# Optimization experiments

Measured on AMD Instinct MI355X. Metric: run time of the kernel, lower is better.

## Reference

```python
import jax, jax.numpy as jnp
import numpy as np

NUM_HEADS = 8
BLOCK = 16
EPS = 1e-5


def setup_inputs() -> dict:
    key = jax.random.key(0)
    ks = jax.random.split(key, 5)
    B, C, H, W = 2, 256, 192, 192
    x = jax.random.normal(ks[0], (B, C, H, W), dtype=jnp.float32)
    s = 1.0 / np.sqrt(C).astype(np.float32)
    Wq = jax.random.normal(ks[1], (C, C), dtype=jnp.float32) * s
    Wk = jax.random.normal(ks[2], (C, C), dtype=jnp.float32) * s
    Wv = jax.random.normal(ks[3], (C, C), dtype=jnp.float32) * s
    Wo = jax.random.normal(ks[4], (C, C), dtype=jnp.float32) * s
    gamma = jnp.ones((C,), dtype=jnp.float32)
    beta = jnp.zeros((C,), dtype=jnp.float32)
    return {"x": x, "Wq": Wq, "Wk": Wk, "Wv": Wv, "Wo": Wo, "gamma": gamma, "beta": beta}


def _to_blocks(t, B, nH, d, H, W, bs):
    # [B, C, H, W] -> [B, nH, n_blocks, bs*bs, d]
    nbh, nbw = H // bs, W // bs
    t = t.reshape(B, nH, d, nbh, bs, nbw, bs)
    t = t.transpose(0, 1, 3, 5, 4, 6, 2)  # B nH nbh nbw bs bs d
    return t.reshape(B, nH, nbh * nbw, bs * bs, d)


def _from_blocks(t, B, nH, d, H, W, bs):
    # [B, nH, n_blocks, bs*bs, d] -> [B, C, H, W]
    nbh, nbw = H // bs, W // bs
    t = t.reshape(B, nH, nbh, nbw, bs, bs, d)
    t = t.transpose(0, 1, 6, 2, 4, 3, 5)  # B nH d nbh bs nbw bs
    return t.reshape(B, nH * d, H, W)


def reference(x, Wq, Wk, Wv, Wo, gamma, beta):
    B, C, H, W = x.shape
    nH, bs = NUM_HEADS, BLOCK
    d = C // nH
    scale = 1.0 / np.float32(np.sqrt(d))

    # 1x1 convs == channel matmuls
    q = jnp.einsum('bchw,oc->bohw', x, Wq)
    k = jnp.einsum('bchw,oc->bohw', x, Wk)
    v = jnp.einsum('bchw,oc->bohw', x, Wv)

    qb = _to_blocks(q, B, nH, d, H, W, bs)
    kb = _to_blocks(k, B, nH, d, H, W, bs)
    vb = _to_blocks(v, B, nH, d, H, W, bs)

    # block-local attention: i,j index the bs*bs pixels inside a block
    scores = jnp.einsum('bnkid,bnkjd->bnkij', qb, kb) * scale
    attn = jax.nn.softmax(scores, axis=-1)
    o = jnp.einsum('bnkij,bnkjd->bnkid', attn, vb)

    o = _from_blocks(o, B, nH, d, H, W, bs)
    o = jnp.einsum('bchw,oc->bohw', o, Wo) + x  # output projection + residual

    # LayerNorm over channels
    mu = jnp.mean(o, axis=1, keepdims=True)
    var = jnp.var(o, axis=1, keepdims=True)
    o = (o - mu) * jax.lax.rsqrt(var + EPS)
    return o * gamma[None, :, None, None] + beta[None, :, None, None]
```

## Files before the change

### kernel.cpp

```cpp
#include <hip/hip_runtime.h>
#include <hip/hip_bf16.h>

namespace {

constexpr int kC    = 256;
constexpr int kH    = 192, kW = 192;
constexpr int kHW   = kH * kW;
constexpr int kNBD  = 12;
constexpr int kNBLK = kNBD * kNBD;

typedef __attribute__((ext_vector_type(8))) short          bf16x8;
typedef __attribute__((ext_vector_type(8))) unsigned short u16x8;
typedef __attribute__((ext_vector_type(4))) unsigned short u16x4;
typedef __attribute__((ext_vector_type(4))) float          f32x4;

__device__ __forceinline__ unsigned short f2bf(float f) {
  union { float f; unsigned u; } x; x.f = f;
  unsigned r = x.u + 0x7fffu + ((x.u >> 16) & 1u);
  return (unsigned short)(r >> 16);
}

__device__ __forceinline__ f32x4 mfma16(bf16x8 a, bf16x8 b, f32x4 c) {
  return __builtin_amdgcn_mfma_f32_16x16x32_bf16(a, b, c, 0, 0, 0);
}

__global__ void k_convw(const float* __restrict__ wq, const float* __restrict__ wk,
                        const float* __restrict__ wv, const float* __restrict__ wo,
                        unsigned short* __restrict__ dst) {
  int i = blockIdx.x * 256 + threadIdx.x;
  const float* s = (blockIdx.y == 0) ? wq : (blockIdx.y == 1) ? wk
                 : (blockIdx.y == 2) ? wv : wo;
  dst[(size_t)blockIdx.y * 65536 + i] = f2bf(s[i]);
}

__global__ __launch_bounds__(256, 3)
void k_qkv(const float* __restrict__ x, const unsigned short* __restrict__ wbf,
           unsigned short* __restrict__ qw, unsigned short* __restrict__ kw,
           unsigned short* __restrict__ vw) {
  __shared__ unsigned short xTs[64 * 256];
  __shared__ unsigned short oT[32 * 264];
  const int tid = threadIdx.x;
  const int w = tid >> 6, l = tid & 63;
  const int m0 = blockIdx.x * 64;
  const int b  = m0 / kHW;
  const int px0 = m0 % kHW;

  {
    const float* xb = x + (size_t)b * kC * kHW + px0;
    #pragma unroll
    for (int i = 0; i < 64; i += 2) {
      const int c = w * 64 + i;
      float f0 = xb[(size_t)c * kHW + l];
      float f1 = xb[(size_t)(c + 1) * kHW + l];
      unsigned pk = (unsigned)f2bf(f0) | ((unsigned)f2bf(f1) << 16);
      const int cb = c >> 3;
      const int col = ((cb ^ (l & 7)) << 3) + (c & 7);
      *(unsigned*)&xTs[l * 256 + col] = pk;
    }
  }
  __syncthreads();

  const int lane = tid & 63;
  const int l15 = lane & 15, l4 = lane >> 4;

  unsigned short* outs[3] = {qw, kw, vw};
  for (int mat = 0; mat < 3; ++mat) {
    const unsigned short* wmat = wbf + (size_t)mat * 65536;
    f32x4 acc[4][4];
    #pragma unroll
    for (int pt = 0; pt < 4; ++pt)
      #pragma unroll
      for (int ot = 0; ot < 4; ++ot)
        acc[pt][ot] = (f32x4){0.f, 0.f, 0.f, 0.f};

    for (int kc = 0; kc < 8; ++kc) {
      bf16x8 bfr[4];
      #pragma unroll
      for (int ot = 0; ot < 4; ++ot)
        bfr[ot] = *(const bf16x8*)&wmat[(size_t)(w * 64 + ot * 16 + l15) * 256 + kc * 32 + l4 * 8];
      #pragma unroll
      for (int pt = 0; pt < 4; ++pt) {
        const int cb = kc * 4 + l4;
        bf16x8 af = *(const bf16x8*)&xTs[(pt * 16 + l15) * 256 + ((cb ^ (l15 & 7)) << 3)];
        #pragma unroll
        for (int ot = 0; ot < 4; ++ot)
          acc[pt][ot] = mfma16(af, bfr[ot], acc[pt][ot]);
      }
    }
    unsigned short* dst = outs[mat] + ((size_t)b * kHW + px0) * 256;
    for (int half = 0; half < 2; ++half) {
      __syncthreads();
      #pragma unroll
      for (int pt2 = 0; pt2 < 2; ++pt2) {
        const int pt = half * 2 + pt2;
        #pragma unroll
        for (int ot = 0; ot < 4; ++ot)
          #pragma unroll
          for (int r = 0; r < 4; ++r)
            oT[(pt2 * 16 + l4 * 4 + r) * 264 + w * 64 + ot * 16 + l15] = f2bf(acc[pt][ot][r]);
      }
      __syncthreads();
      const int row = tid >> 3, ocb = tid & 7;
      #pragma unroll
      for (int k2 = 0; k2 < 4; ++k2) {
        u16x8 vv = *(const u16x8*)&oT[row * 264 + ocb * 32 + k2 * 8];
        *(u16x8*)&dst[(size_t)(half * 32 + row) * 256 + ocb * 32 + k2 * 8] = vv;
      }
    }
  }
}

__global__ __launch_bounds__(512, 2)
void k_attn(const unsigned short* __restrict__ qw, const unsigned short* __restrict__ kw,
            const unsigned short* __restrict__ vw, unsigned short* __restrict__ ow) {
  __shared__ unsigned short P[256][264];
  __shared__ unsigned short T[32][264];
  const int tid = threadIdx.x;
  int bx = blockIdx.x;
  const int blk = bx % kNBLK; bx /= kNBLK;
  const int head = bx & 7; const int b = bx >> 3;
  const int bh = blk / kNBD, bw = blk % kNBD;
  const int px00 = bh * 16 * kW + bw * 16;
  const size_t base = ((size_t)b * kHW) * 256 + head * 32;

  {
    const int j = tid >> 1, half = tid & 1;
    const int px = px00 + (j >> 4) * kW + (j & 15);
    const unsigned short* vp = vw + base + (size_t)px * 256 + half * 16;
    u16x8 a = *(const u16x8*)&vp[0];
    u16x8 c = *(const u16x8*)&vp[8];
    #pragma unroll
    for (int e = 0; e < 8; ++e) {
      T[half * 16 + e][j]     = a[e];
      T[half * 16 + 8 + e][j] = c[e];
    }
  }

  const int lane = tid & 63, wave = tid >> 6;
  const int l15 = lane & 15, l4 = lane >> 4;
  const f32x4 fz = {0.f, 0.f, 0.f, 0.f};

  bf16x8 qfr[2];
  #pragma unroll
  for (int it = 0; it < 2; ++it) {
    const int i  = wave * 32 + it * 16 + l15;
    const int px = px00 + (i >> 4) * kW + (i & 15);
    qfr[it] = *(const bf16x8*)&qw[base + (size_t)px * 256 + l4 * 8];
  }
  f32x4 s[16][2];
  #pragma unroll
  for (int jt = 0; jt < 16; ++jt) {
    const int px = px00 + jt * kW + l15;
    bf16x8 kf = *(const bf16x8*)&kw[base + (size_t)px * 256 + l4 * 8];
    s[jt][0] = mfma16(kf, qfr[0], fz);
    s[jt][1] = mfma16(kf, qfr[1], fz);
  }

  const float sc = 0.17677669529663687f;
  #pragma unroll
  for (int it = 0; it < 2; ++it) {
    float m = -3.0e38f;
    #pragma unroll
    for (int jt = 0; jt < 16; ++jt)
      #pragma unroll
      for (int r = 0; r < 4; ++r)
        m = fmaxf(m, s[jt][it][r]);
    m = fmaxf(m, __shfl_xor(m, 16));
    m = fmaxf(m, __shfl_xor(m, 32));
    float su = 0.f;
    #pragma unroll
    for (int jt = 0; jt < 16; ++jt)
      #pragma unroll
      for (int r = 0; r < 4; ++r) {
        float e = __expf((s[jt][it][r] - m) * sc);
        s[jt][it][r] = e;
        su += e;
      }
    su += __shfl_xor(su, 16);
    su += __shfl_xor(su, 32);
    const float inv = 1.f / su;
    const int i = wave * 32 + it * 16 + l15;
    #pragma unroll
    for (int jt = 0; jt < 16; ++jt) {
      u16x4 pk;
      #pragma unroll
      for (int r = 0; r < 4; ++r) pk[r] = f2bf(s[jt][it][r] * inv);
      *(u16x4*)&P[i][jt * 16 + l4 * 4] = pk;
    }
  }
  __syncthreads();

  f32x4 oa[2][2];
  oa[0][0] = fz; oa[0][1] = fz; oa[1][0] = fz; oa[1][1] = fz;
  #pragma unroll
  for (int kt = 0; kt < 8; ++kt) {
    bf16x8 av0 = *(const bf16x8*)&T[l15][kt * 32 + l4 * 8];
    bf16x8 av1 = *(const bf16x8*)&T[16 + l15][kt * 32 + l4 * 8];
    bf16x8 bp0 = *(const bf16x8*)&P[wave * 32 + l15][kt * 32 + l4 * 8];
    bf16x8 bp1 = *(const bf16x8*)&P[wave * 32 + 16 + l15][kt * 32 + l4 * 8];
    oa[0][0] = mfma16(av0, bp0, oa[0][0]);
    oa[0][1] = mfma16(av0, bp1, oa[0][1]);
    oa[1][0] = mfma16(av1, bp0, oa[1][0]);
    oa[1][1] = mfma16(av1, bp1, oa[1][1]);
  }
  __syncthreads();
  #pragma unroll
  for (int ddt = 0; ddt < 2; ++ddt)
    #pragma unroll
    for (int it = 0; it < 2; ++it)
      #pragma unroll
      for (int r = 0; r < 4; ++r)
        T[ddt * 16 + l4 * 4 + r][wave * 32 + it * 16 + l15] = f2bf(oa[ddt][it][r]);
  __syncthreads();
  {
    const int i = tid >> 1, half = tid & 1;
    const int px = px00 + (i >> 4) * kW + (i & 15);
    u16x8 w0, w1;
    #pragma unroll
    for (int e = 0; e < 8; ++e) {
      w0[e] = T[half * 16 + e][i];
      w1[e] = T[half * 16 + 8 + e][i];
    }
    unsigned short* op = ow + base + (size_t)px * 256 + half * 16;
    *(u16x8*)&op[0] = w0;
    *(u16x8*)&op[8] = w1;
  }
}

__global__ __launch_bounds__(256, 3)
void k_proj_ln(const unsigned short* __restrict__ oatt, const unsigned short* __restrict__ wo,
               const float* __restrict__ x, const float* __restrict__ gamma,
               const float* __restrict__ beta, float* __restrict__ out) {
  __shared__ float pa[4][64], pb[4][64];
  const int tid = threadIdx.x, w = tid >> 6, lane = tid & 63;
  const int l15 = lane & 15, l4 = lane >> 4;
  const int m0 = blockIdx.x * 64;
  const int b = m0 / kHW, px0 = m0 % kHW;

  f32x4 acc[4][4];
  #pragma unroll
  for (int ot = 0; ot < 4; ++ot)
    #pragma unroll
    for (int pt = 0; pt < 4; ++pt)
      acc[ot][pt] = (f32x4){0.f, 0.f, 0.f, 0.f};

  const unsigned short* ob = oatt + ((size_t)b * kHW + px0) * 256;
  for (int kc = 0; kc < 8; ++kc) {
    bf16x8 bfr[4];
    #pragma unroll
    for (int pt = 0; pt < 4; ++pt)
      bfr[pt] = *(const bf16x8*)&ob[(size_t)(pt * 16 + l15) * 256 + kc * 32 + l4 * 8];
    #pragma unroll
    for (int ot = 0; ot < 4; ++ot) {
      bf16x8 af = *(const bf16x8*)&wo[(size_t)(w * 64 + ot * 16 + l15) * 256 + kc * 32 + l4 * 8];
      #pragma unroll
      for (int pt = 0; pt < 4; ++pt)
        acc[ot][pt] = mfma16(af, bfr[pt], acc[ot][pt]);
    }
  }

  const float* xb = x + (size_t)b * kC * kHW + px0;
  float s1[4] = {0.f, 0.f, 0.f, 0.f}, s2[4] = {0.f, 0.f, 0.f, 0.f};
  #pragma unroll
  for (int ot = 0; ot < 4; ++ot)
    #pragma unroll
    for (int r = 0; r < 4; ++r) {
      const int oc = w * 64 + ot * 16 + l4 * 4 + r;
      #pragma unroll
      for (int pt = 0; pt < 4; ++pt) {
        float v = acc[ot][pt][r] + xb[(size_t)oc * kHW + pt * 16 + l15];
        acc[ot][pt][r] = v;
        s1[pt] += v;
        s2[pt] += v * v;
      }
    }
  #pragma unroll
  for (int pt = 0; pt < 4; ++pt) {
    s1[pt] += __shfl_xor(s1[pt], 16);
    s1[pt] += __shfl_xor(s1[pt], 32);
    s2[pt] += __shfl_xor(s2[pt], 16);
    s2[pt] += __shfl_xor(s2[pt], 32);
  }
  if (l4 == 0) {
    #pragma unroll
    for (int pt = 0; pt < 4; ++pt) {
      pa[w][pt * 16 + l15] = s1[pt];
      pb[w][pt * 16 + l15] = s2[pt];
    }
  }
  __syncthreads();
  float mean[4], rstd[4];
  #pragma unroll
  for (int pt = 0; pt < 4; ++pt) {
    const int px = pt * 16 + l15;
    float a = pa[0][px] + pa[1][px] + pa[2][px] + pa[3][px];
    float q = pb[0][px] + pb[1][px] + pb[2][px] + pb[3][px];
    mean[pt] = a * (1.f / 256.f);
    float var = q * (1.f / 256.f) - mean[pt] * mean[pt];
    rstd[pt] = rsqrtf(var + 1e-5f);
  }
  float* outb = out + (size_t)b * kC * kHW + px0;
  #pragma unroll
  for (int ot = 0; ot < 4; ++ot)
    #pragma unroll
    for (int r = 0; r < 4; ++r) {
      const int oc = w * 64 + ot * 16 + l4 * 4 + r;
      const float g = gamma[oc], be = beta[oc];
      #pragma unroll
      for (int pt = 0; pt < 4; ++pt)
        outb[(size_t)oc * kHW + pt * 16 + l15] = (acc[ot][pt][r] - mean[pt]) * rstd[pt] * g + be;
    }
}

}

extern "C" void kernel_launch(void* const* d_in, const int* in_sizes, int n_in,
                              void* d_out, int out_size, void* d_ws, size_t ws_size,
                              hipStream_t stream) {
  const float* x     = (const float*)d_in[0];
  const float* Wq    = (const float*)d_in[1];
  const float* Wk    = (const float*)d_in[2];
  const float* Wv    = (const float*)d_in[3];
  const float* Wo    = (const float*)d_in[4];
  const float* gamma = (const float*)d_in[5];
  const float* beta  = (const float*)d_in[6];
  float* out = (float*)d_out;

  const int nbatch = 2;
  const size_t per = (size_t)nbatch * kHW * 256;

  unsigned short* wbf = (unsigned short*)d_ws;
  unsigned short* qws = wbf + 4 * 65536;
  unsigned short* kws = qws + per;
  unsigned short* vws = kws + per;
  unsigned short* ows = qws;

  k_convw<<<dim3(256, 4), 256, 0, stream>>>(Wq, Wk, Wv, Wo, wbf);
  k_qkv<<<(nbatch * kHW) / 64, 256, 0, stream>>>(x, wbf, qws, kws, vws);
  k_attn<<<nbatch * 8 * kNBLK, 512, 0, stream>>>(qws, kws, vws, ows);
  k_proj_ln<<<(nbatch * kHW) / 64, 256, 0, stream>>>(ows, wbf + 3 * 65536, x, gamma, beta, out);
}
```

Baseline: 241.6 us.

## Swap MFMA operands in QKV GEMM to write outputs directly without LDS staging

Result: slower. 370.3 us (+53.3%).

```diff
diff --git a/kernel.cpp b/kernel.cpp
--- a/kernel.cpp
+++ b/kernel.cpp
@@ -33,12 +33,11 @@
   dst[(size_t)blockIdx.y * 65536 + i] = f2bf(s[i]);
 }
 
-__global__ __launch_bounds__(256, 3)
+__global__ __launch_bounds__(256, 4)
 void k_qkv(const float* __restrict__ x, const unsigned short* __restrict__ wbf,
            unsigned short* __restrict__ qw, unsigned short* __restrict__ kw,
            unsigned short* __restrict__ vw) {
   __shared__ unsigned short xTs[64 * 256];
-  __shared__ unsigned short oT[32 * 264];
   const int tid = threadIdx.x;
   const int w = tid >> 6, l = tid & 63;
   const int m0 = blockIdx.x * 64;
@@ -60,53 +59,45 @@
   }
   __syncthreads();
 
-  const int lane = tid & 63;
-  const int l15 = lane & 15, l4 = lane >> 4;
-
-  unsigned short* outs[3] = {qw, kw, vw};
+  const int l15 = l & 15, l4 = l >> 4;
+
   for (int mat = 0; mat < 3; ++mat) {
     const unsigned short* wmat = wbf + (size_t)mat * 65536;
     f32x4 acc[4][4];
     #pragma unroll
-    for (int pt = 0; pt < 4; ++pt)
+    for (int ot = 0; ot < 4; ++ot)
+      #pragma unroll
+      for (int pt = 0; pt < 4; ++pt)
+        acc[ot][pt] = (f32x4){0.f, 0.f, 0.f, 0.f};
+
+    #pragma unroll
+    for (int kc = 0; kc < 8; ++kc) {
+      bf16x8 af[4], bf[4];
       #pragma unroll
       for (int ot = 0; ot < 4; ++ot)
-        acc[pt][ot] = (f32x4){0.f, 0.f, 0.f, 0.f};
-
-    for (int kc = 0; kc < 8; ++kc) {
-      bf16x8 bfr[4];
-      #pragma unroll
-      for (int ot = 0; ot < 4; ++ot)
-        bfr[ot] = *(const bf16x8*)&wmat[(size_t)(w * 64 + ot * 16 + l15) * 256 + kc * 32 + l4 * 8];
+        af[ot] = *(const bf16x8*)&wmat[(size_t)(w * 64 + ot * 16 + l15) * 256 + kc * 32 + l4 * 8];
       #pragma unroll
       for (int pt = 0; pt < 4; ++pt) {
         const int cb = kc * 4 + l4;
-        bf16x8 af = *(const bf16x8*)&xTs[(pt * 16 + l15) * 256 + ((cb ^ (l15 & 7)) << 3)];
+        bf[pt] = *(const bf16x8*)&xTs[(pt * 16 + l15) * 256 + ((cb ^ (l15 & 7)) << 3)];
+      }
+      #pragma unroll
+      for (int ot = 0; ot < 4; ++ot)
         #pragma unroll
-        for (int ot = 0; ot < 4; ++ot)
-          acc[pt][ot] = mfma16(af, bfr[ot], acc[pt][ot]);
+        for (int pt = 0; pt < 4; ++pt)
+          acc[ot][pt] = mfma16(af[ot], bf[pt], acc[ot][pt]);
+    }
+
+    unsigned short* dst = (mat == 0 ? qw : (mat == 1 ? kw : vw)) + ((size_t)b * kHW + px0) * 256;
+    #pragma unroll
+    for (int ot = 0; ot < 4; ++ot)
+      #pragma unroll
+      for (int pt = 0; pt < 4; ++pt) {
+        u16x4 pk;
+        #pragma unroll
+        for (int r = 0; r < 4; ++r) pk[r] = f2bf(acc[ot][pt][r]);
+        *(u16x4*)&dst[(size_t)(pt * 16 + l15) * 256 + w * 64 + ot * 16 + l4 * 4] = pk;
       }
-    }
-    unsigned short* dst = outs[mat] + ((size_t)b * kHW + px0) * 256;
-    for (int half = 0; half < 2; ++half) {
-      __syncthreads();
-      #pragma unroll
-      for (int pt2 = 0; pt2 < 2; ++pt2) {
-        const int pt = half * 2 + pt2;
-        #pragma unroll
-        for (int ot = 0; ot < 4; ++ot)
-          #pragma unroll
-          for (int r = 0; r < 4; ++r)
-            oT[(pt2 * 16 + l4 * 4 + r) * 264 + w * 64 + ot * 16 + l15] = f2bf(acc[pt][ot][r]);
-      }
-      __syncthreads();
-      const int row = tid >> 3, ocb = tid & 7;
-      #pragma unroll
-      for (int k2 = 0; k2 < 4; ++k2) {
-        u16x8 vv = *(const u16x8*)&oT[row * 264 + ocb * 32 + k2 * 8];
-        *(u16x8*)&dst[(size_t)(half * 32 + row) * 256 + ocb * 32 + k2 * 8] = vv;
-      }
-    }
   }
 }
 
```
